# Kernel tuning notes

Measured on AMD Instinct MI355X. Metric: run time of the kernel, lower is better.

The kernel has to match this reference:

```python
import jax, jax.numpy as jnp
import numpy as np

NUM_STEPS = 5


def setup_inputs() -> dict:
    key = jax.random.key(0)
    ks = jax.random.split(key, 12)
    B, N, H, E, A = 8, 1024, 64, 2, 8
    initial_state = jax.random.normal(ks[0], (B, N, H), dtype=jnp.float32)
    annotation = jax.random.normal(ks[1], (B, N, A), dtype=jnp.float32)
    # sparse-ish positive adjacency, scaled so matmul outputs don't saturate gates
    adj_matrix = jax.random.uniform(ks[2], (B, N, 2 * N * E), dtype=jnp.float32) * 0.01
    s = 0.05
    W_edge = jax.random.normal(ks[3], (H, H * E), dtype=jnp.float32) * s
    b_edge = jax.random.normal(ks[4], (H * E,), dtype=jnp.float32) * s
    W_gate = jax.random.normal(ks[5], (3 * H, H), dtype=jnp.float32) * s
    b_gate = jax.random.normal(ks[6], (H,), dtype=jnp.float32) * s
    W_hid = jax.random.normal(ks[7], (H + A, H), dtype=jnp.float32) * s
    b_hid = jax.random.normal(ks[8], (H,), dtype=jnp.float32) * s
    W_out = jax.random.normal(ks[9], (H, 1), dtype=jnp.float32) * s
    b_out = jax.random.normal(ks[10], (1,), dtype=jnp.float32) * s
    return dict(initial_state=initial_state, annotation=annotation, adj_matrix=adj_matrix,
                W_edge=W_edge, b_edge=b_edge, W_gate=W_gate, b_gate=b_gate,
                W_hid=W_hid, b_hid=b_hid, W_out=W_out, b_out=b_out)


def reference(initial_state, annotation, adj_matrix, W_edge, b_edge,
              W_gate, b_gate, W_hid, b_hid, W_out, b_out):
    B, N, H = initial_state.shape
    E = W_edge.shape[1] // H
    boundary = N * E
    A_in = adj_matrix[:, :, :boundary]   # [B, N, N*E]
    A_out = adj_matrix[:, :, boundary:]  # [B, N, N*E]

    h = initial_state
    for _ in range(NUM_STEPS):
        # Linear(H, H*E) then view/transpose to [B, N*E, H].
        # Original computes incoming_edge and outgoing_edge with the SAME
        # linear on the SAME input -> identical tensors; compute once.
        edge = jnp.einsum('bnh,he->bne', h, W_edge) + b_edge      # [B, N, H*E]
        edge = edge.reshape(B, N, H, E).transpose(0, 3, 1, 2).reshape(B, N * E, H)
        a_in = jnp.matmul(A_in, edge)    # [B, N, H]
        a_out = jnp.matmul(A_out, edge)  # [B, N, H]
        a = jnp.concatenate([a_in, a_out, h], axis=2)             # [B, N, 3H]
        # update and reset use the same gate linear -> equal; compute once.
        z = jax.nn.sigmoid(jnp.einsum('bnk,kh->bnh', a, W_gate) + b_gate)
        a_r = jnp.concatenate([a_in, a_out, z * h], axis=2)
        h_tilde = jnp.tanh(jnp.einsum('bnk,kh->bnh', a_r, W_gate) + b_gate)
        h = (1.0 - z) * h + z * h_tilde

    # task_id not in {18, 19}: node-level output head
    ha = jnp.concatenate([h, annotation], axis=2)                 # [B, N, H+A]
    out = jnp.tanh(jnp.einsum('bnk,kh->bnh', ha, W_hid) + b_hid)  # [B, N, H]
    out = (jnp.einsum('bnh,ho->bno', out, W_out) + b_out).sum(axis=2)  # [B, N]
    return out
```

## Files before the change

### kernel.cpp

```cpp
#include <hip/hip_runtime.h>
#include <math.h>

#define BN    8
#define NN    1024
#define HH    64
#define ADIM  8
#define STEPS 5
#define K2    2048
#define ROWS  (BN*NN)

typedef __attribute__((ext_vector_type(8))) short bf16x8;
typedef __attribute__((ext_vector_type(4))) float f32x4;

__device__ __forceinline__ unsigned short f2bf(float f) {
    unsigned int u = __float_as_uint(f);
    u += 0x7FFF + ((u >> 16) & 1);
    return (unsigned short)(u >> 16);
}
__device__ __forceinline__ float bf2f(unsigned short h) {
    return __uint_as_float(((unsigned int)h) << 16);
}
__device__ __forceinline__ float ftanh(float x) {
    float e = __expf(2.f * x);
    return 1.f - 2.f / (e + 1.f);
}

__device__ __forceinline__ void lgkm_barrier() {
    asm volatile("s_waitcnt lgkmcnt(0)" ::: "memory");
    __builtin_amdgcn_s_barrier();
    asm volatile("" ::: "memory");
}


__global__ __launch_bounds__(256) void conv_adj(
    const float* __restrict__ in, unsigned short* __restrict__ out)
{
    __shared__ unsigned short tl[8][520];
    int bid = blockIdx.x;
    int kg = bid & 7;
    int ng = (bid >> 3) & 63;
    int d  = (bid >> 9) & 1;
    int b  = bid >> 10;
    int t = threadIdx.x;

    const float* src = in + ((size_t)(b * 1024 + ng * 16)) * 4096 + d * 2048 + kg * 256;
    #pragma unroll
    for (int it = 0; it < 4; ++it) {
        int u = it * 256 + t;
        int r = u >> 6, c4 = u & 63;
        float4 v = *(const float4*)(src + (size_t)r * 4096 + c4 * 4);
        int k = c4 * 4;
        int kb = k >> 5, kk = k & 31;
        ushort4 o;
        o.x = f2bf(v.x); o.y = f2bf(v.y); o.z = f2bf(v.z); o.w = f2bf(v.w);
        *(ushort4*)&tl[kb][r * 32 + kk] = o;
    }
    __syncthreads();

    unsigned short* dst = out + (((size_t)(b * 2 + d) * 64 + kg * 8) * 64 + ng) * 512;
    #pragma unroll
    for (int it = 0; it < 4; ++it) {
        int u = it * 256 + t;
        int kb = u >> 7, wo = u & 127;
        *(ushort4*)(dst + (size_t)kb * 32768 + wo * 4) = *(const ushort4*)&tl[kb][wo * 4];
    }
}

__global__ __launch_bounds__(256) void prep_pack(
    const float* __restrict__ Wg, const float* __restrict__ We,
    unsigned short* __restrict__ wgp, unsigned short* __restrict__ wep)
{
    int t = blockIdx.x * 256 + threadIdx.x;
    if (t < 12288) {
        int k = t >> 6, c = t & 63;
        float v = Wg[t];
        unsigned short hi = f2bf(v);
        unsigned short lo = f2bf(v - bf2f(hi));
        wgp[(size_t)c * 192 + k] = hi;
        wgp[(size_t)(64 + c) * 192 + k] = lo;
    } else if (t < 20480) {
        int u = t - 12288;
        int k = u >> 7, c = u & 127;
        float v = We[u];
        unsigned short hi = f2bf(v);
        unsigned short lo = f2bf(v - bf2f(hi));
        wep[(size_t)c * 64 + k] = hi;
        wep[(size_t)(128 + c) * 64 + k] = lo;
    }
}

__global__ __launch_bounds__(256) void init_kernel(
    const float* __restrict__ init_state,
    const float* __restrict__ We, const float* __restrict__ be,
    float* __restrict__ h_ws, unsigned short* __restrict__ edge_t)
{
    __shared__ float h_lds[4][65];
    int t = threadIdx.x;
    int r = t >> 6, hp = t & 63;
    int row = blockIdx.x * 4 + r;
    float hv = init_state[(size_t)row * 64 + hp];
    h_ws[(size_t)row * 64 + hp] = hv;
    h_lds[r][hp] = hv;
    __syncthreads();
    int b = row >> 10, n = row & 1023;
    #pragma unroll
    for (int e = 0; e < 2; ++e) {
        float acc = be[hp * 2 + e];
        #pragma unroll 8
        for (int c = 0; c < 64; ++c)
            acc += h_lds[r][c] * We[c * 128 + hp * 2 + e];
        edge_t[((size_t)b * 64 + hp) * K2 + e * NN + n] = f2bf(acc);
    }
}

__global__ __launch_bounds__(512) void step_kernel(
    const unsigned short* __restrict__ adjf,
    const unsigned short* __restrict__ ein,
    unsigned short* __restrict__ eout,
    float* __restrict__ h_ws,
    const unsigned short* __restrict__ wgp,
    const unsigned short* __restrict__ wep,
    const float* __restrict__ bg,
    const float* __restrict__ be,
    const float* __restrict__ ann,
    const float* __restrict__ Wh, const float* __restrict__ bh,
    const float* __restrict__ Wo, const float* __restrict__ bo,
    float* __restrict__ out,
    int mode)
{
    __shared__ __attribute__((aligned(16))) unsigned short Bs[2][64][264];
    __shared__ __attribute__((aligned(16))) unsigned short Xhi[32][200];
    __shared__ __attribute__((aligned(16))) unsigned short Xlo[32][200];
    __shared__ __attribute__((aligned(16))) float          hf [32][68];
    __shared__ __attribute__((aligned(16))) unsigned short HNhi[32][72];
    __shared__ __attribute__((aligned(16))) unsigned short HNlo[32][72];

    int t  = threadIdx.x;
    int b  = blockIdx.x >> 5;
    int mt = blockIdx.x & 31;
    int n0 = mt * 32;
    size_t hbase = ((size_t)(b * NN + n0)) * 64;

    int lane = t & 63, w = t >> 6, l15 = lane & 15, q = lane >> 4;
    int dir = w >> 2, rh = (w >> 1) & 1, kc = w & 1;
    int nb  = mt * 2 + rh;

    const unsigned short* A2 = adjf
        + (((size_t)(b * 2 + dir) * 64 + kc * 4) * 64 + nb) * 512 + l15 * 32 + q * 8;

    int srow[4], scol[4];
    const unsigned short* sptr[4];
    #pragma unroll
    for (int i = 0; i < 4; ++i) {
        int u = i * 512 + t;
        srow[i] = u >> 5; scol[i] = (u & 31) * 8;
        sptr[i] = ein + ((size_t)b * 64 + srow[i]) * K2 + scol[i];
    }

    int hr = t >> 4, hcg = (t & 15) * 4;
    float4 hv4 = *(const float4*)(h_ws + hbase + (size_t)hr * 64 + hcg);

    uint4 gA[4], gB[4];
    #pragma unroll
    for (int i = 0; i < 4; ++i) gA[i] = *(const uint4*)(sptr[i]);
    #pragma unroll
    for (int i = 0; i < 4; ++i) gB[i] = *(const uint4*)(sptr[i] + 256);
    bf16x8 afA[4], afB[4];
    #pragma unroll
    for (int ks = 0; ks < 4; ++ks)
        afA[ks] = *(const bf16x8*)(A2 + (size_t)ks * 32768);
    #pragma unroll
    for (int ks = 0; ks < 4; ++ks)
        afB[ks] = *(const bf16x8*)(A2 + (size_t)(8 + ks) * 32768);

    {
        float vv[4] = {hv4.x, hv4.y, hv4.z, hv4.w};
        #pragma unroll
        for (int j = 0; j < 4; ++j) {
            float hv = vv[j];
            unsigned short hi = f2bf(hv), lo = f2bf(hv - bf2f(hi));
            Xhi[hr][128 + hcg + j] = hi;
            Xlo[hr][128 + hcg + j] = lo;
            hf[hr][hcg + j] = hv;
        }
    }

    #pragma unroll
    for (int i = 0; i < 4; ++i)
        *(uint4*)&Bs[0][srow[i]][scol[i]] = gA[i];
    lgkm_barrier();

    f32x4 acc[4];
    #pragma unroll
    for (int ct = 0; ct < 4; ++ct) acc[ct] = (f32x4){0.f, 0.f, 0.f, 0.f};

    #pragma unroll
    for (int c = 0; c < 8; ++c) {
        const int par = c & 1;
        if (c < 6) {
            #pragma unroll
            for (int i = 0; i < 4; ++i) {
                uint4 v = *(const uint4*)(sptr[i] + (c + 2) * 256);
                if (par == 0) gA[i] = v; else gB[i] = v;
            }
        }
        #pragma unroll
        for (int ks = 0; ks < 4; ++ks) {
            bf16x8 a = (par == 0) ? afA[ks] : afB[ks];
            #pragma unroll
            for (int ct = 0; ct < 4; ++ct) {
                bf16x8 bfr = *(const bf16x8*)&Bs[par][ct * 16 + l15][kc * 128 + ks * 32 + q * 8];
                acc[ct] = __builtin_amdgcn_mfma_f32_16x16x32_bf16(a, bfr, acc[ct], 0, 0, 0);
            }
        }
        if (c < 6) {
            #pragma unroll
            for (int ks = 0; ks < 4; ++ks) {
                bf16x8 v = *(const bf16x8*)(A2 + (size_t)((c + 2) * 8 + ks) * 32768);
                if (par == 0) afA[ks] = v; else afB[ks] = v;
            }
        }
        if (c < 7) {
            #pragma unroll
            for (int i = 0; i < 4; ++i) {
                uint4 v = (par == 0) ? gB[i] : gA[i];
                *(uint4*)&Bs[par ^ 1][srow[i]][scol[i]] = v;
            }
        }
        lgkm_barrier();
    }

    float (*red)[16][68] = (float (*)[16][68])(&Bs[0][0][0]);
    int gg = w >> 1;
    if (kc == 1) {
        #pragma unroll
        for (int ct = 0; ct < 4; ++ct)
            #pragma unroll
            for (int i = 0; i < 4; ++i)
                red[gg][q * 4 + i][ct * 16 + l15] = acc[ct][i];
    }
    __syncthreads();
    if (kc == 0) {
        #pragma unroll
        for (int ct = 0; ct < 4; ++ct)
            #pragma unroll
            for (int i = 0; i < 4; ++i) {
                float v = acc[ct][i] + red[gg][q * 4 + i][ct * 16 + l15];
                unsigned short hi = f2bf(v), lo = f2bf(v - bf2f(hi));
                int r  = rh * 16 + q * 4 + i;
                int cc2 = dir * 64 + ct * 16 + l15;
                Xhi[r][cc2] = hi;
                Xlo[r][cc2] = lo;
            }
    }
    __syncthreads();

    int mg = w & 1, cg16 = w >> 1;
    int arow = mg * 16 + l15;
    int cc = cg16 * 16 + l15;
    const unsigned short* wcol = wgp + (size_t)cc * 192;
    f32x4 as = (f32x4){0.f, 0.f, 0.f, 0.f}, az;

    #pragma unroll
    for (int ks = 0; ks < 4; ++ks) {
        bf16x8 ah = *(const bf16x8*)&Xhi[arow][ks * 32 + q * 8];
        bf16x8 al = *(const bf16x8*)&Xlo[arow][ks * 32 + q * 8];
        const unsigned short* wb = wcol + ks * 32 + q * 8;
        bf16x8 bh2 = *(const bf16x8*)wb;
        bf16x8 bl2 = *(const bf16x8*)(wb + 64 * 192);
        as = __builtin_amdgcn_mfma_f32_16x16x32_bf16(ah, bh2, as, 0, 0, 0);
        as = __builtin_amdgcn_mfma_f32_16x16x32_bf16(ah, bl2, as, 0, 0, 0);
        as = __builtin_amdgcn_mfma_f32_16x16x32_bf16(al, bh2, as, 0, 0, 0);
    }
    az = as;
    #pragma unroll
    for (int ks = 4; ks < 6; ++ks) {
        bf16x8 ah = *(const bf16x8*)&Xhi[arow][ks * 32 + q * 8];
        bf16x8 al = *(const bf16x8*)&Xlo[arow][ks * 32 + q * 8];
        const unsigned short* wb = wcol + ks * 32 + q * 8;
        bf16x8 bh2 = *(const bf16x8*)wb;
        bf16x8 bl2 = *(const bf16x8*)(wb + 64 * 192);
        az = __builtin_amdgcn_mfma_f32_16x16x32_bf16(ah, bh2, az, 0, 0, 0);
        az = __builtin_amdgcn_mfma_f32_16x16x32_bf16(ah, bl2, az, 0, 0, 0);
        az = __builtin_amdgcn_mfma_f32_16x16x32_bf16(al, bh2, az, 0, 0, 0);
    }
    __syncthreads();

    float zv[4], hv[4];
    float bgv = bg[cc];
    #pragma unroll
    for (int i = 0; i < 4; ++i) {
        int r = mg * 16 + q * 4 + i;
        float z = 1.f / (1.f + __expf(-(az[i] + bgv)));
        float h = hf[r][cc];
        zv[i] = z; hv[i] = h;
        float zh = z * h;
        unsigned short hi = f2bf(zh), lo = f2bf(zh - bf2f(hi));
        Xhi[r][128 + cc] = hi;
        Xlo[r][128 + cc] = lo;
    }
    __syncthreads();

    #pragma unroll
    for (int ks = 4; ks < 6; ++ks) {
        bf16x8 ah = *(const bf16x8*)&Xhi[arow][ks * 32 + q * 8];
        bf16x8 al = *(const bf16x8*)&Xlo[arow][ks * 32 + q * 8];
        const unsigned short* wb = wcol + ks * 32 + q * 8;
        bf16x8 bh2 = *(const bf16x8*)wb;
        bf16x8 bl2 = *(const bf16x8*)(wb + 64 * 192);
        as = __builtin_amdgcn_mfma_f32_16x16x32_bf16(ah, bh2, as, 0, 0, 0);
        as = __builtin_amdgcn_mfma_f32_16x16x32_bf16(ah, bl2, as, 0, 0, 0);
        as = __builtin_amdgcn_mfma_f32_16x16x32_bf16(al, bh2, as, 0, 0, 0);
    }

    #pragma unroll
    for (int i = 0; i < 4; ++i) {
        int r = mg * 16 + q * 4 + i;
        float ht = ftanh(as[i] + bgv);
        float z  = zv[i];
        float hn = (1.f - z) * hv[i] + z * ht;
        if (mode == 0) {
            h_ws[hbase + (size_t)r * 64 + cc] = hn;
            unsigned short hi = f2bf(hn), lo = f2bf(hn - bf2f(hi));
            HNhi[r][cc] = hi;
            HNlo[r][cc] = lo;
        } else {
            hf[r][cc] = hn;
        }
    }
    __syncthreads();

    if (mode == 0) {
        int me = w & 1, cb2 = (w >> 1) * 2;
        int erow = me * 16 + l15;
        f32x4 ae[2];
        ae[0] = ae[1] = (f32x4){0.f, 0.f, 0.f, 0.f};
        #pragma unroll
        for (int ks = 0; ks < 2; ++ks) {
            bf16x8 ah = *(const bf16x8*)&HNhi[erow][ks * 32 + q * 8];
            bf16x8 al = *(const bf16x8*)&HNlo[erow][ks * 32 + q * 8];
            #pragma unroll
            for (int p = 0; p < 2; ++p) {
                int ec = (cb2 + p) * 16 + l15;
                const unsigned short* wb = wep + (size_t)ec * 64 + ks * 32 + q * 8;
                bf16x8 bh2 = *(const bf16x8*)wb;
                bf16x8 bl2 = *(const bf16x8*)(wb + 128 * 64);
                ae[p] = __builtin_amdgcn_mfma_f32_16x16x32_bf16(ah, bh2, ae[p], 0, 0, 0);
                ae[p] = __builtin_amdgcn_mfma_f32_16x16x32_bf16(ah, bl2, ae[p], 0, 0, 0);
                ae[p] = __builtin_amdgcn_mfma_f32_16x16x32_bf16(al, bh2, ae[p], 0, 0, 0);
            }
        }
        #pragma unroll
        for (int p = 0; p < 2; ++p) {
            int ec = (cb2 + p) * 16 + l15;
            float bev = be[ec];
            int hp2 = ec >> 1, e = ec & 1;
            size_t ebase = ((size_t)b * 64 + hp2) * K2 + (size_t)e * NN
                         + n0 + me * 16 + q * 4;
            ushort4 ev;
            ev.x = f2bf(ae[p][0] + bev);
            ev.y = f2bf(ae[p][1] + bev);
            ev.z = f2bf(ae[p][2] + bev);
            ev.w = f2bf(ae[p][3] + bev);
            *(ushort4*)(eout + ebase) = ev;
        }
    } else {
        int r = t >> 4, hq = (t & 15) * 4;
        int row = b * NN + n0 + r;
        float av[ADIM];
        #pragma unroll
        for (int j = 0; j < ADIM; ++j) av[j] = ann[(size_t)row * ADIM + j];
        float ac2[4];
        #pragma unroll
        for (int i = 0; i < 4; ++i) ac2[i] = bh[hq + i];
        #pragma unroll 8
        for (int k = 0; k < 64; ++k) {
            float hv2 = hf[r][k];
            float4 wv = *(const float4*)&Wh[k * 64 + hq];
            ac2[0] += hv2 * wv.x; ac2[1] += hv2 * wv.y;
            ac2[2] += hv2 * wv.z; ac2[3] += hv2 * wv.w;
        }
        #pragma unroll
        for (int k = 0; k < ADIM; ++k) {
            float4 wv = *(const float4*)&Wh[(64 + k) * 64 + hq];
            ac2[0] += av[k] * wv.x; ac2[1] += av[k] * wv.y;
            ac2[2] += av[k] * wv.z; ac2[3] += av[k] * wv.w;
        }
        float v = 0.f;
        #pragma unroll
        for (int i = 0; i < 4; ++i)
            v += ftanh(ac2[i]) * Wo[hq + i];
        #pragma unroll
        for (int m = 8; m; m >>= 1) v += __shfl_xor(v, m, 64);
        if ((t & 15) == 0) out[row] = v + bo[0];
    }
}

extern "C" void kernel_launch(void* const* d_in, const int* in_sizes, int n_in,
                              void* d_out, int out_size, void* d_ws, size_t ws_size,
                              hipStream_t stream) {
    const float* init_state = (const float*)d_in[0];
    const float* ann = (const float*)d_in[1];
    const float* adj = (const float*)d_in[2];
    const float* We  = (const float*)d_in[3];
    const float* be  = (const float*)d_in[4];
    const float* Wg  = (const float*)d_in[5];
    const float* bg  = (const float*)d_in[6];
    const float* Wh  = (const float*)d_in[7];
    const float* bh  = (const float*)d_in[8];
    const float* Wo  = (const float*)d_in[9];
    const float* bo  = (const float*)d_in[10];
    float* out = (float*)d_out;

    char* wsb = (char*)d_ws;
    unsigned short* adjf   = (unsigned short*)wsb;
    unsigned short* edge_a = (unsigned short*)(wsb + 67108864);
    unsigned short* edge_b = (unsigned short*)(wsb + 69206016);
    float*          h_ws   = (float*)(wsb + 71303168);
    unsigned short* wgp    = (unsigned short*)(wsb + 73400320);
    unsigned short* wep    = (unsigned short*)(wsb + 73449472);

    conv_adj<<<dim3(8192), dim3(256), 0, stream>>>(adj, adjf);
    prep_pack<<<dim3(80), dim3(256), 0, stream>>>(Wg, We, wgp, wep);
    init_kernel<<<dim3(ROWS / 4), dim3(256), 0, stream>>>(init_state, We, be, h_ws, edge_a);
    for (int s = 0; s < STEPS; ++s) {
        const unsigned short* ein = (s & 1) ? edge_b : edge_a;
        unsigned short* eo        = (s & 1) ? edge_a : edge_b;
        step_kernel<<<dim3(256), dim3(512), 0, stream>>>(
            adjf, ein, eo, h_ws, wgp, wep, bg, be,
            ann, Wh, bh, Wo, bo, out, (s == STEPS - 1) ? 1 : 0);
    }
}
```

Baseline: 377.4 us.

## Halve step-kernel row tile to 16 nodes, doubling grid to 512 blocks

Each step block now handles 16 nodes instead of 32. Its 8 waves split by direction and output column tile and walk the full K range, so the cross-wave K-split reduction goes away. The grid doubles to 512 blocks to fill more of the CUs on the device, and launch bounds request 4 blocks per CU. In exchange, each edge tile is reloaded by twice as many blocks, which raises global and L2 traffic, and only half the waves do work in the gate phase.

```diff
diff --git a/kernel.cpp b/kernel.cpp
--- a/kernel.cpp
+++ b/kernel.cpp
@@ -113,7 +113,7 @@
     }
 }
 
-__global__ __launch_bounds__(512) void step_kernel(
+__global__ __launch_bounds__(512, 4) void step_kernel(
     const unsigned short* __restrict__ adjf,
     const unsigned short* __restrict__ ein,
     unsigned short* __restrict__ eout,
@@ -128,52 +128,46 @@
     float* __restrict__ out,
     int mode)
 {
-    __shared__ __attribute__((aligned(16))) unsigned short Bs[2][64][264];
-    __shared__ __attribute__((aligned(16))) unsigned short Xhi[32][200];
-    __shared__ __attribute__((aligned(16))) unsigned short Xlo[32][200];
-    __shared__ __attribute__((aligned(16))) float          hf [32][68];
-    __shared__ __attribute__((aligned(16))) unsigned short HNhi[32][72];
-    __shared__ __attribute__((aligned(16))) unsigned short HNlo[32][72];
+    __shared__ __attribute__((aligned(16))) unsigned short Bs[2][64][136];
+    __shared__ __attribute__((aligned(16))) unsigned short Xhi[16][200];
+    __shared__ __attribute__((aligned(16))) unsigned short Xlo[16][200];
+    __shared__ __attribute__((aligned(16))) float          hf [16][68];
+    __shared__ __attribute__((aligned(16))) unsigned short HNhi[16][72];
+    __shared__ __attribute__((aligned(16))) unsigned short HNlo[16][72];
 
     int t  = threadIdx.x;
-    int b  = blockIdx.x >> 5;
-    int mt = blockIdx.x & 31;
-    int n0 = mt * 32;
+    int b  = blockIdx.x >> 6;
+    int mt = blockIdx.x & 63;
+    int n0 = mt * 16;
     size_t hbase = ((size_t)(b * NN + n0)) * 64;
 
     int lane = t & 63, w = t >> 6, l15 = lane & 15, q = lane >> 4;
-    int dir = w >> 2, rh = (w >> 1) & 1, kc = w & 1;
-    int nb  = mt * 2 + rh;
+    int dir = w >> 2, ct = w & 3;
+    int ct16 = ct * 16;
 
     const unsigned short* A2 = adjf
-        + (((size_t)(b * 2 + dir) * 64 + kc * 4) * 64 + nb) * 512 + l15 * 32 + q * 8;
-
-    int srow[4], scol[4];
-    const unsigned short* sptr[4];
-    #pragma unroll
-    for (int i = 0; i < 4; ++i) {
-        int u = i * 512 + t;
-        srow[i] = u >> 5; scol[i] = (u & 31) * 8;
-        sptr[i] = ein + ((size_t)b * 64 + srow[i]) * K2 + scol[i];
-    }
+        + (((size_t)(b * 2 + dir) * 64) * 64 + mt) * 512 + l15 * 32 + q * 8;
+
+    int srow = t >> 3, scol = (t & 7) * 16;
+    const unsigned short* sptr = ein + ((size_t)b * 64 + srow) * K2 + scol;
 
     int hr = t >> 4, hcg = (t & 15) * 4;
-    float4 hv4 = *(const float4*)(h_ws + hbase + (size_t)hr * 64 + hcg);
-
-    uint4 gA[4], gB[4];
-    #pragma unroll
-    for (int i = 0; i < 4; ++i) gA[i] = *(const uint4*)(sptr[i]);
-    #pragma unroll
-    for (int i = 0; i < 4; ++i) gB[i] = *(const uint4*)(sptr[i] + 256);
+    float4 hv4;
+    if (t < 256) hv4 = *(const float4*)(h_ws + hbase + (size_t)hr * 64 + hcg);
+
+    uint4 sA0 = *(const uint4*)(sptr);
+    uint4 sA1 = *(const uint4*)(sptr + 8);
+    uint4 sB0 = *(const uint4*)(sptr + 128);
+    uint4 sB1 = *(const uint4*)(sptr + 136);
     bf16x8 afA[4], afB[4];
     #pragma unroll
     for (int ks = 0; ks < 4; ++ks)
         afA[ks] = *(const bf16x8*)(A2 + (size_t)ks * 32768);
     #pragma unroll
     for (int ks = 0; ks < 4; ++ks)
-        afB[ks] = *(const bf16x8*)(A2 + (size_t)(8 + ks) * 32768);
-
-    {
+        afB[ks] = *(const bf16x8*)(A2 + (size_t)(4 + ks) * 32768);
+
+    if (t < 256) {
         float vv[4] = {hv4.x, hv4.y, hv4.z, hv4.w};
         #pragma unroll
         for (int j = 0; j < 4; ++j) {
@@ -185,186 +179,159 @@
         }
     }
 
-    #pragma unroll
-    for (int i = 0; i < 4; ++i)
-        *(uint4*)&Bs[0][srow[i]][scol[i]] = gA[i];
+    *(uint4*)&Bs[0][srow][scol]     = sA0;
+    *(uint4*)&Bs[0][srow][scol + 8] = sA1;
     lgkm_barrier();
 
-    f32x4 acc[4];
-    #pragma unroll
-    for (int ct = 0; ct < 4; ++ct) acc[ct] = (f32x4){0.f, 0.f, 0.f, 0.f};
-
-    #pragma unroll
-    for (int c = 0; c < 8; ++c) {
+    f32x4 acc = (f32x4){0.f, 0.f, 0.f, 0.f};
+
+    #pragma unroll
+    for (int c = 0; c < 16; ++c) {
         const int par = c & 1;
-        if (c < 6) {
-            #pragma unroll
-            for (int i = 0; i < 4; ++i) {
-                uint4 v = *(const uint4*)(sptr[i] + (c + 2) * 256);
-                if (par == 0) gA[i] = v; else gB[i] = v;
-            }
+        if (c < 14) {
+            uint4 v0 = *(const uint4*)(sptr + (c + 2) * 128);
+            uint4 v1 = *(const uint4*)(sptr + (c + 2) * 128 + 8);
+            if (par == 0) { sA0 = v0; sA1 = v1; } else { sB0 = v0; sB1 = v1; }
         }
         #pragma unroll
         for (int ks = 0; ks < 4; ++ks) {
             bf16x8 a = (par == 0) ? afA[ks] : afB[ks];
-            #pragma unroll
-            for (int ct = 0; ct < 4; ++ct) {
-                bf16x8 bfr = *(const bf16x8*)&Bs[par][ct * 16 + l15][kc * 128 + ks * 32 + q * 8];
-                acc[ct] = __builtin_amdgcn_mfma_f32_16x16x32_bf16(a, bfr, acc[ct], 0, 0, 0);
-            }
-        }
-        if (c < 6) {
+            bf16x8 bfr = *(const bf16x8*)&Bs[par][ct16 + l15][ks * 32 + q * 8];
+            acc = __builtin_amdgcn_mfma_f32_16x16x32_bf16(a, bfr, acc, 0, 0, 0);
+        }
+        if (c < 14) {
             #pragma unroll
             for (int ks = 0; ks < 4; ++ks) {
-                bf16x8 v = *(const bf16x8*)(A2 + (size_t)((c + 2) * 8 + ks) * 32768);
+                bf16x8 v = *(const bf16x8*)(A2 + (size_t)((c + 2) * 4 + ks) * 32768);
                 if (par == 0) afA[ks] = v; else afB[ks] = v;
             }
         }
-        if (c < 7) {
-            #pragma unroll
-            for (int i = 0; i < 4; ++i) {
-                uint4 v = (par == 0) ? gB[i] : gA[i];
-                *(uint4*)&Bs[par ^ 1][srow[i]][scol[i]] = v;
+        if (c < 15) {
+            uint4 w0 = (par == 0) ? sB0 : sA0;
+            uint4 w1 = (par == 0) ? sB1 : sA1;
+            *(uint4*)&Bs[par ^ 1][srow][scol]     = w0;
+            *(uint4*)&Bs[par ^ 1][srow][scol + 8] = w1;
+        }
+        lgkm_barrier();
+    }
+
+    {
+        int cc2 = dir * 64 + ct16 + l15;
+        #pragma unroll
+        for (int i = 0; i < 4; ++i) {
+            float v = acc[i];
+            unsigned short hi = f2bf(v), lo = f2bf(v - bf2f(hi));
+            int r = q * 4 + i;
+            Xhi[r][cc2] = hi;
+            Xlo[r][cc2] = lo;
+        }
+    }
+    __syncthreads();
+
+    int cc = (w & 3) * 16 + l15;
+    f32x4 as = (f32x4){0.f, 0.f, 0.f, 0.f}, az = as;
+    float bgv = 0.f;
+    if (w < 4) {
+        const unsigned short* wcol = wgp + (size_t)cc * 192;
+        bgv = bg[cc];
+        #pragma unroll
+        for (int ks = 0; ks < 4; ++ks) {
+            bf16x8 ah = *(const bf16x8*)&Xhi[l15][ks * 32 + q * 8];
+            bf16x8 al = *(const bf16x8*)&Xlo[l15][ks * 32 + q * 8];
+            const unsigned short* wb = wcol + ks * 32 + q * 8;
+            bf16x8 bh2 = *(const bf16x8*)wb;
+            bf16x8 bl2 = *(const bf16x8*)(wb + 64 * 192);
+            as = __builtin_amdgcn_mfma_f32_16x16x32_bf16(ah, bh2, as, 0, 0, 0);
+            as = __builtin_amdgcn_mfma_f32_16x16x32_bf16(ah, bl2, as, 0, 0, 0);
+            as = __builtin_amdgcn_mfma_f32_16x16x32_bf16(al, bh2, as, 0, 0, 0);
+        }
+        az = as;
+        #pragma unroll
+        for (int ks = 4; ks < 6; ++ks) {
+            bf16x8 ah = *(const bf16x8*)&Xhi[l15][ks * 32 + q * 8];
+            bf16x8 al = *(const bf16x8*)&Xlo[l15][ks * 32 + q * 8];
+            const unsigned short* wb = wcol + ks * 32 + q * 8;
+            bf16x8 bh2 = *(const bf16x8*)wb;
+            bf16x8 bl2 = *(const bf16x8*)(wb + 64 * 192);
+            az = __builtin_amdgcn_mfma_f32_16x16x32_bf16(ah, bh2, az, 0, 0, 0);
+            az = __builtin_amdgcn_mfma_f32_16x16x32_bf16(ah, bl2, az, 0, 0, 0);
+            az = __builtin_amdgcn_mfma_f32_16x16x32_bf16(al, bh2, az, 0, 0, 0);
+        }
+    }
+    __syncthreads();
+
+    float zv[4], hv[4];
+    if (w < 4) {
+        #pragma unroll
+        for (int i = 0; i < 4; ++i) {
+            int r = q * 4 + i;
+            float z = 1.f / (1.f + __expf(-(az[i] + bgv)));
+            float h = hf[r][cc];
+            zv[i] = z; hv[i] = h;
+            float zh = z * h;
+            unsigned short hi = f2bf(zh), lo = f2bf(zh - bf2f(hi));
+            Xhi[r][128 + cc] = hi;
+            Xlo[r][128 + cc] = lo;
+        }
+    }
+    __syncthreads();
+
+    if (w < 4) {
+        const unsigned short* wcol = wgp + (size_t)cc * 192;
+        #pragma unroll
+        for (int ks = 4; ks < 6; ++ks) {
+            bf16x8 ah = *(const bf16x8*)&Xhi[l15][ks * 32 + q * 8];
+            bf16x8 al = *(const bf16x8*)&Xlo[l15][ks * 32 + q * 8];
+            const unsigned short* wb = wcol + ks * 32 + q * 8;
+            bf16x8 bh2 = *(const bf16x8*)wb;
+            bf16x8 bl2 = *(const bf16x8*)(wb + 64 * 192);
+            as = __builtin_amdgcn_mfma_f32_16x16x32_bf16(ah, bh2, as, 0, 0, 0);
+            as = __builtin_amdgcn_mfma_f32_16x16x32_bf16(ah, bl2, as, 0, 0, 0);
+            as = __builtin_amdgcn_mfma_f32_16x16x32_bf16(al, bh2, as, 0, 0, 0);
+        }
+        #pragma unroll
+        for (int i = 0; i < 4; ++i) {
+            int r = q * 4 + i;
+            float ht = ftanh(as[i] + bgv);
+            float z  = zv[i];
+            float hn = (1.f - z) * hv[i] + z * ht;
+            if (mode == 0) {
+                h_ws[hbase + (size_t)r * 64 + cc] = hn;
+                unsigned short hi = f2bf(hn), lo = f2bf(hn - bf2f(hi));
+                HNhi[r][cc] = hi;
+                HNlo[r][cc] = lo;
+            } else {
+                hf[r][cc] = hn;
             }
         }
-        lgkm_barrier();
-    }
-
-    float (*red)[16][68] = (float (*)[16][68])(&Bs[0][0][0]);
-    int gg = w >> 1;
-    if (kc == 1) {
-        #pragma unroll
-        for (int ct = 0; ct < 4; ++ct)
-            #pragma unroll
-            for (int i = 0; i < 4; ++i)
-                red[gg][q * 4 + i][ct * 16 + l15] = acc[ct][i];
-    }
-    __syncthreads();
-    if (kc == 0) {
-        #pragma unroll
-        for (int ct = 0; ct < 4; ++ct)
-            #pragma unroll
-            for (int i = 0; i < 4; ++i) {
-                float v = acc[ct][i] + red[gg][q * 4 + i][ct * 16 + l15];
-                unsigned short hi = f2bf(v), lo = f2bf(v - bf2f(hi));
-                int r  = rh * 16 + q * 4 + i;
-                int cc2 = dir * 64 + ct * 16 + l15;
-                Xhi[r][cc2] = hi;
-                Xlo[r][cc2] = lo;
-            }
-    }
-    __syncthreads();
-
-    int mg = w & 1, cg16 = w >> 1;
-    int arow = mg * 16 + l15;
-    int cc = cg16 * 16 + l15;
-    const unsigned short* wcol = wgp + (size_t)cc * 192;
-    f32x4 as = (f32x4){0.f, 0.f, 0.f, 0.f}, az;
-
-    #pragma unroll
-    for (int ks = 0; ks < 4; ++ks) {
-        bf16x8 ah = *(const bf16x8*)&Xhi[arow][ks * 32 + q * 8];
-        bf16x8 al = *(const bf16x8*)&Xlo[arow][ks * 32 + q * 8];
-        const unsigned short* wb = wcol + ks * 32 + q * 8;
-        bf16x8 bh2 = *(const bf16x8*)wb;
-        bf16x8 bl2 = *(const bf16x8*)(wb + 64 * 192);
-        as = __builtin_amdgcn_mfma_f32_16x16x32_bf16(ah, bh2, as, 0, 0, 0);
-        as = __builtin_amdgcn_mfma_f32_16x16x32_bf16(ah, bl2, as, 0, 0, 0);
-        as = __builtin_amdgcn_mfma_f32_16x16x32_bf16(al, bh2, as, 0, 0, 0);
-    }
-    az = as;
-    #pragma unroll
-    for (int ks = 4; ks < 6; ++ks) {
-        bf16x8 ah = *(const bf16x8*)&Xhi[arow][ks * 32 + q * 8];
-        bf16x8 al = *(const bf16x8*)&Xlo[arow][ks * 32 + q * 8];
-        const unsigned short* wb = wcol + ks * 32 + q * 8;
-        bf16x8 bh2 = *(const bf16x8*)wb;
-        bf16x8 bl2 = *(const bf16x8*)(wb + 64 * 192);
-        az = __builtin_amdgcn_mfma_f32_16x16x32_bf16(ah, bh2, az, 0, 0, 0);
-        az = __builtin_amdgcn_mfma_f32_16x16x32_bf16(ah, bl2, az, 0, 0, 0);
-        az = __builtin_amdgcn_mfma_f32_16x16x32_bf16(al, bh2, az, 0, 0, 0);
-    }
-    __syncthreads();
-
-    float zv[4], hv[4];
-    float bgv = bg[cc];
-    #pragma unroll
-    for (int i = 0; i < 4; ++i) {
-        int r = mg * 16 + q * 4 + i;
-        float z = 1.f / (1.f + __expf(-(az[i] + bgv)));
-        float h = hf[r][cc];
-        zv[i] = z; hv[i] = h;
-        float zh = z * h;
-        unsigned short hi = f2bf(zh), lo = f2bf(zh - bf2f(hi));
-        Xhi[r][128 + cc] = hi;
-        Xlo[r][128 + cc] = lo;
-    }
-    __syncthreads();
-
-    #pragma unroll
-    for (int ks = 4; ks < 6; ++ks) {
-        bf16x8 ah = *(const bf16x8*)&Xhi[arow][ks * 32 + q * 8];
-        bf16x8 al = *(const bf16x8*)&Xlo[arow][ks * 32 + q * 8];
-        const unsigned short* wb = wcol + ks * 32 + q * 8;
-        bf16x8 bh2 = *(const bf16x8*)wb;
-        bf16x8 bl2 = *(const bf16x8*)(wb + 64 * 192);
-        as = __builtin_amdgcn_mfma_f32_16x16x32_bf16(ah, bh2, as, 0, 0, 0);
-        as = __builtin_amdgcn_mfma_f32_16x16x32_bf16(ah, bl2, as, 0, 0, 0);
-        as = __builtin_amdgcn_mfma_f32_16x16x32_bf16(al, bh2, as, 0, 0, 0);
-    }
-
-    #pragma unroll
-    for (int i = 0; i < 4; ++i) {
-        int r = mg * 16 + q * 4 + i;
-        float ht = ftanh(as[i] + bgv);
-        float z  = zv[i];
-        float hn = (1.f - z) * hv[i] + z * ht;
-        if (mode == 0) {
-            h_ws[hbase + (size_t)r * 64 + cc] = hn;
-            unsigned short hi = f2bf(hn), lo = f2bf(hn - bf2f(hi));
-            HNhi[r][cc] = hi;
-            HNlo[r][cc] = lo;
-        } else {
-            hf[r][cc] = hn;
-        }
     }
     __syncthreads();
 
     if (mode == 0) {
-        int me = w & 1, cb2 = (w >> 1) * 2;
-        int erow = me * 16 + l15;
-        f32x4 ae[2];
-        ae[0] = ae[1] = (f32x4){0.f, 0.f, 0.f, 0.f};
+        int ec = w * 16 + l15;
+        const unsigned short* wb0 = wep + (size_t)ec * 64;
+        f32x4 ae = (f32x4){0.f, 0.f, 0.f, 0.f};
         #pragma unroll
         for (int ks = 0; ks < 2; ++ks) {
-            bf16x8 ah = *(const bf16x8*)&HNhi[erow][ks * 32 + q * 8];
-            bf16x8 al = *(const bf16x8*)&HNlo[erow][ks * 32 + q * 8];
-            #pragma unroll
-            for (int p = 0; p < 2; ++p) {
-                int ec = (cb2 + p) * 16 + l15;
-                const unsigned short* wb = wep + (size_t)ec * 64 + ks * 32 + q * 8;
-                bf16x8 bh2 = *(const bf16x8*)wb;
-                bf16x8 bl2 = *(const bf16x8*)(wb + 128 * 64);
-                ae[p] = __builtin_amdgcn_mfma_f32_16x16x32_bf16(ah, bh2, ae[p], 0, 0, 0);
-                ae[p] = __builtin_amdgcn_mfma_f32_16x16x32_bf16(ah, bl2, ae[p], 0, 0, 0);
-                ae[p] = __builtin_amdgcn_mfma_f32_16x16x32_bf16(al, bh2, ae[p], 0, 0, 0);
-            }
-        }
-        #pragma unroll
-        for (int p = 0; p < 2; ++p) {
-            int ec = (cb2 + p) * 16 + l15;
-            float bev = be[ec];
-            int hp2 = ec >> 1, e = ec & 1;
-            size_t ebase = ((size_t)b * 64 + hp2) * K2 + (size_t)e * NN
-                         + n0 + me * 16 + q * 4;
-            ushort4 ev;
-            ev.x = f2bf(ae[p][0] + bev);
-            ev.y = f2bf(ae[p][1] + bev);
-            ev.z = f2bf(ae[p][2] + bev);
-            ev.w = f2bf(ae[p][3] + bev);
-            *(ushort4*)(eout + ebase) = ev;
-        }
-    } else {
+            bf16x8 ah = *(const bf16x8*)&HNhi[l15][ks * 32 + q * 8];
+            bf16x8 al = *(const bf16x8*)&HNlo[l15][ks * 32 + q * 8];
+            const unsigned short* wb = wb0 + ks * 32 + q * 8;
+            bf16x8 bh2 = *(const bf16x8*)wb;
+            bf16x8 bl2 = *(const bf16x8*)(wb + 128 * 64);
+            ae = __builtin_amdgcn_mfma_f32_16x16x32_bf16(ah, bh2, ae, 0, 0, 0);
+            ae = __builtin_amdgcn_mfma_f32_16x16x32_bf16(ah, bl2, ae, 0, 0, 0);
+            ae = __builtin_amdgcn_mfma_f32_16x16x32_bf16(al, bh2, ae, 0, 0, 0);
+        }
+        float bev = be[ec];
+        int hp2 = ec >> 1, e = ec & 1;
+        size_t ebase = ((size_t)b * 64 + hp2) * K2 + (size_t)e * NN + n0 + q * 4;
+        ushort4 ev;
+        ev.x = f2bf(ae[0] + bev);
+        ev.y = f2bf(ae[1] + bev);
+        ev.z = f2bf(ae[2] + bev);
+        ev.w = f2bf(ae[3] + bev);
+        *(ushort4*)(eout + ebase) = ev;
+    } else if (t < 256) {
         int r = t >> 4, hq = (t & 15) * 4;
         int row = b * NN + n0 + r;
         float av[ADIM];
@@ -426,7 +393,7 @@
     for (int s = 0; s < STEPS; ++s) {
         const unsigned short* ein = (s & 1) ? edge_b : edge_a;
         unsigned short* eo        = (s & 1) ? edge_a : edge_b;
-        step_kernel<<<dim3(256), dim3(512), 0, stream>>>(
+        step_kernel<<<dim3(512), dim3(512), 0, stream>>>(
             adjf, ein, eo, h_ws, wgp, wep, bg, be,
             ann, Wh, bh, Wo, bo, out, (s == STEPS - 1) ? 1 : 0);
     }
```

Measured after the change: 395.0 us. 1.05x slower.
